# Performance work log

Measured on AMD Instinct MI355X. Metric: run time of the kernel, lower is better.

The kernel has to match this reference:

```python
import jax, jax.numpy as jnp
import numpy as np

B, S, D_IN, D_OUT = 8, 4096, 1024, 1024
R_F, R_M, R_S = 8, 32, 64
R_TOT = R_F + R_M + R_S  # 104
HID = 64
ALPHA = 1.0


def setup_inputs() -> dict:
    key = jax.random.key(0)
    ks = jax.random.split(key, 10)
    inp = {
        "x": jax.random.normal(ks[0], (B, S, D_IN), dtype=jnp.float32),
        # fresh memory state after reset_memory(): zeros of shape [batch, r_*]
        "mem_fast": jnp.zeros((B, R_F), dtype=jnp.float32),
        "mem_medium": jnp.zeros((B, R_M), dtype=jnp.float32),
        "mem_slow": jnp.zeros((B, R_S), dtype=jnp.float32),
        # frozen base nn.Linear
        "base_w": jax.random.normal(ks[1], (D_OUT, D_IN), dtype=jnp.float32) / np.sqrt(D_IN),
        "base_b": jax.random.normal(ks[2], (D_OUT,), dtype=jnp.float32) * 0.01,
        # LoRA projections: proj_down kaiming-ish, proj_up zero-init per _init_weights
        "pd_w": jax.random.normal(ks[3], (R_TOT, D_IN), dtype=jnp.float32) / np.sqrt(D_IN),
        "pu_w": jax.random.normal(ks[4], (D_OUT, R_TOT), dtype=jnp.float32) * 0.01,
        # gate_net: Linear(D_IN, HID) -> GELU -> Linear(HID, 3) -> Softmax
        "g1_w": jax.random.normal(ks[5], (HID, D_IN), dtype=jnp.float32) / np.sqrt(D_IN),
        "g1_b": jnp.zeros((HID,), dtype=jnp.float32),
        "g2_w": jax.random.normal(ks[6], (3, HID), dtype=jnp.float32) / np.sqrt(HID),
        "g2_b": jnp.zeros((3,), dtype=jnp.float32),
    }
    return inp


def reference(x, mem_fast, mem_medium, mem_slow, base_w, base_b,
              pd_w, pu_w, g1_w, g1_b, g2_w, g2_b):
    # base linear: [B,S,D_out]
    base_out = jnp.einsum("bsd,od->bso", x, base_w) + base_b
    # down projection: [B,S,R_TOT]
    proj = jnp.einsum("bsd,rd->bsr", x, pd_w)
    # per-timescale multiplicative modulation by recurrent memory state
    # (split -> (1+mem)*proj -> concat) == concat memories once
    mem = jnp.concatenate([mem_fast, mem_medium, mem_slow], axis=-1)  # [B,R_TOT]
    modulated = proj * (1.0 + mem[:, None, :])
    # gate_net: Linear -> GELU(exact) -> Linear -> softmax over 3 timescales
    h = jax.nn.gelu(jnp.einsum("bsd,hd->bsh", x, g1_w) + g1_b, approximate=False)
    gates = jax.nn.softmax(jnp.einsum("bsh,gh->bsg", h, g2_w) + g2_b, axis=-1)
    gate_scale = jnp.mean(gates, axis=-1, keepdims=True)  # [B,S,1]
    # up projection and residual combine
    lora_out = jnp.einsum("bsr,or->bso", modulated, pu_w)
    output = base_out + ALPHA * lora_out * gate_scale
    return output
```

## Files before the change

kernel.cpp:

```cpp
#include <hip/hip_runtime.h>
#include <stdint.h>


typedef unsigned short ushort_t;
typedef unsigned short us8 __attribute__((ext_vector_type(8)));
typedef short short8 __attribute__((ext_vector_type(8)));
typedef float f32x4 __attribute__((ext_vector_type(4)));

__device__ __forceinline__ ushort_t f2b(float f) {
  union { float f; uint32_t i; } v; v.f = f;
  uint32_t lsb = (v.i >> 16) & 1u;
  v.i += 0x7fffu + lsb;
  return (ushort_t)(v.i >> 16);
}

__device__ __forceinline__ void async16(const void* g, void* l) {
  __builtin_amdgcn_global_load_lds(
      (const __attribute__((address_space(1))) void*)g,
      (__attribute__((address_space(3))) void*)l, 16, 0, 0);
}

__global__ __launch_bounds__(256) void convert_x(const float* __restrict__ x,
                                                 ushort_t* __restrict__ xb) {
  const int flat = blockIdx.x;
  const int b = flat & 7;
  const int c = flat >> 3;
  const size_t i = (((size_t)b * 2048 + c) * 256 + threadIdx.x) * 8;
  f32x4 a0 = *(const f32x4*)(x + i);
  f32x4 a1 = *(const f32x4*)(x + i + 4);
  us8 o;
#pragma unroll
  for (int j = 0; j < 4; j++) { o[j] = f2b(a0[j]); o[4 + j] = f2b(a1[j]); }
  *(us8*)(xb + i) = o;
}

__global__ __launch_bounds__(128) void prep(const float* __restrict__ base_w,
                                            const float* __restrict__ pu_w,
                                            const float* __restrict__ pd_w,
                                            const float* __restrict__ mf,
                                            const float* __restrict__ mm,
                                            const float* __restrict__ ms,
                                            ushort_t* __restrict__ W0,
                                            ushort_t* __restrict__ Weff,
                                            int* __restrict__ flags) {
  const int o = blockIdx.x, y = blockIdx.y, t = threadIdx.x;
  __shared__ float spu[104];
  __shared__ int sflag;
  ushort_t* dst;

  if (y == 0) {
    if (t < 104) spu[t] = pu_w[o * 104 + t] * (1.0f / 3.0f);
    dst = W0 + o * 1024;
    __syncthreads();
  } else {
    const int b = y - 1;
    if (t == 0) sflag = 0;
    __syncthreads();
    float mv = 0.0f;
    if (t < 104) {
      mv = (t < 8) ? mf[b * 8 + t]
         : (t < 40) ? mm[b * 32 + (t - 8)]
                    : ms[b * 64 + (t - 40)];
      if (mv != 0.0f) sflag = 1;
      spu[t] = pu_w[o * 104 + t] * (1.0f + mv) * (1.0f / 3.0f);
    }
    __syncthreads();
    if (o == 0 && t == 0) flags[b] = sflag;
    if (!sflag) return;
    dst = Weff + ((size_t)b << 20) + o * 1024;
  }

  const int d0 = t * 8;
  float acc[8];
  f32x4 b0 = *(const f32x4*)(base_w + o * 1024 + d0);
  f32x4 b1 = *(const f32x4*)(base_w + o * 1024 + d0 + 4);
#pragma unroll
  for (int j = 0; j < 4; j++) { acc[j] = b0[j]; acc[4 + j] = b1[j]; }
  for (int r = 0; r < 104; r++) {
    f32x4 p0 = *(const f32x4*)(pd_w + r * 1024 + d0);
    f32x4 p1 = *(const f32x4*)(pd_w + r * 1024 + d0 + 4);
    float s = spu[r];
#pragma unroll
    for (int j = 0; j < 4; j++) { acc[j] += s * p0[j]; acc[4 + j] += s * p1[j]; }
  }
  us8 ov;
#pragma unroll
  for (int j = 0; j < 8; j++) ov[j] = f2b(acc[j]);
  *(us8*)(dst + d0) = ov;
}

__global__ __launch_bounds__(512, 2) void gemm256(
    const ushort_t* __restrict__ xb, const float* __restrict__ base_b,
    const ushort_t* __restrict__ W0, const ushort_t* __restrict__ Weff,
    const int* __restrict__ flags, float* __restrict__ out) {
  const int flat = blockIdx.x;
  const int b  = flat & 7;
  const int i  = flat >> 3;
  const int bm = i >> 2;
  const int bn = i & 3;

  const ushort_t* W = flags[b] ? (Weff + ((size_t)b << 20)) : W0;

  __shared__ __align__(16) char lds[4 * 32768];

  const int t = threadIdx.x;
  const int w = t >> 6, l = t & 63;
  const int wr = w >> 2, wc = w & 3;
  const int row16 = l & 15, quad = l >> 4;

  const int srow = w * 16 + (l >> 2);
  const int scol = (((l & 3) ^ ((l >> 3) & 3))) * 8;
  const ushort_t* gA = xb + (((size_t)b * 4096 + bm * 256 + srow) << 10) + scol;
  const ushort_t* gB = W + (((size_t)(bn * 256 + srow)) << 10) + scol;

  const int qsw = (quad ^ ((row16 >> 1) & 3)) * 16;
  const int aoff = (wr * 128 + row16) * 64 + qsw;
  const int boff = 16384 + (wc * 64 + row16) * 64 + qsw;

#define STAGE_A(kt)                                                       \
  {                                                                       \
    const int bi_ = (kt) & 3;                                             \
    const ushort_t* g_ = gA + (kt) * 32;                                  \
    char* d_ = lds + bi_ * 32768 + w * 1024;                              \
    async16(g_, d_);                                                      \
    async16(g_ + (128 << 10), d_ + 8192);                                 \
  }
#define STAGE_B(kt)                                                       \
  {                                                                       \
    const int bi_ = (kt) & 3;                                             \
    const ushort_t* g_ = gB + (kt) * 32;                                  \
    char* d_ = lds + bi_ * 32768 + 16384 + w * 1024;                      \
    async16(g_, d_);                                                      \
    async16(g_ + (128 << 10), d_ + 8192);                                 \
  }

  f32x4 acc[8][4] = {};

  STAGE_A(0) STAGE_B(0) STAGE_A(1) STAGE_B(1)
  asm volatile("s_waitcnt vmcnt(4)" ::: "memory");
  __builtin_amdgcn_s_barrier();

  for (int kt = 0; kt < 32; ++kt) {
    const char* base = lds + (kt & 3) * 32768;

    short8 af[8];
#pragma unroll
    for (int mi = 0; mi < 8; ++mi)
      af[mi] = *(const short8*)(base + aoff + mi * 1024);
    short8 bf0 = *(const short8*)(base + boff);
    short8 bf1 = *(const short8*)(base + boff + 1024);
    if (kt < 30) STAGE_A(kt + 2)
    __builtin_amdgcn_s_barrier();
    __builtin_amdgcn_s_setprio(1);
#pragma unroll
    for (int mi = 0; mi < 8; ++mi) {
      acc[mi][0] = __builtin_amdgcn_mfma_f32_16x16x32_bf16(af[mi], bf0, acc[mi][0], 0, 0, 0);
      acc[mi][1] = __builtin_amdgcn_mfma_f32_16x16x32_bf16(af[mi], bf1, acc[mi][1], 0, 0, 0);
    }
    __builtin_amdgcn_s_setprio(0);
    __builtin_amdgcn_s_barrier();

    short8 bf2 = *(const short8*)(base + boff + 2048);
    short8 bf3 = *(const short8*)(base + boff + 3072);
    if (kt < 30) STAGE_B(kt + 2)
    __builtin_amdgcn_s_barrier();
    __builtin_amdgcn_s_setprio(1);
#pragma unroll
    for (int mi = 0; mi < 8; ++mi) {
      acc[mi][2] = __builtin_amdgcn_mfma_f32_16x16x32_bf16(af[mi], bf2, acc[mi][2], 0, 0, 0);
      acc[mi][3] = __builtin_amdgcn_mfma_f32_16x16x32_bf16(af[mi], bf3, acc[mi][3], 0, 0, 0);
    }
    __builtin_amdgcn_s_setprio(0);

    if (kt < 30) {
      asm volatile("s_waitcnt vmcnt(4)" ::: "memory");
    } else if (kt == 30) {
      asm volatile("s_waitcnt vmcnt(0)" ::: "memory");
    }
    __builtin_amdgcn_s_barrier();
  }

#pragma unroll
  for (int ni = 0; ni < 4; ++ni) {
    const int col = bn * 256 + wc * 64 + ni * 16 + row16;
    const float bb = base_b[col];
#pragma unroll
    for (int mi = 0; mi < 8; ++mi) {
      const int row = bm * 256 + wr * 128 + mi * 16 + quad * 4;
      float* po = out + (((size_t)b * 4096 + row) << 10) + col;
#pragma unroll
      for (int i2 = 0; i2 < 4; ++i2)
        po[(size_t)i2 << 10] = acc[mi][ni][i2] + bb;
    }
  }
#undef STAGE_A
#undef STAGE_B
}

extern "C" void kernel_launch(void* const* d_in, const int* in_sizes, int n_in,
                              void* d_out, int out_size, void* d_ws, size_t ws_size,
                              hipStream_t stream) {
  const float* x  = (const float*)d_in[0];
  const float* mf = (const float*)d_in[1];
  const float* mm = (const float*)d_in[2];
  const float* ms = (const float*)d_in[3];
  const float* base_w = (const float*)d_in[4];
  const float* base_b = (const float*)d_in[5];
  const float* pd_w = (const float*)d_in[6];
  const float* pu_w = (const float*)d_in[7];

  char* ws = (char*)d_ws;
  int* flags     = (int*)ws;
  ushort_t* W0   = (ushort_t*)(ws + 4096);
  ushort_t* xb   = (ushort_t*)(ws + 4096 + (2u << 20));
  ushort_t* Weff = (ushort_t*)(ws + 4096 + (2u << 20) + (64u << 20));

  prep<<<dim3(1024, 9), 128, 0, stream>>>(base_w, pu_w, pd_w, mf, mm, ms,
                                          W0, Weff, flags);
  convert_x<<<16384, 256, 0, stream>>>(x, xb);
  gemm256<<<512, 512, 0, stream>>>(xb, base_b, W0, Weff, flags, (float*)d_out);
}
```

Baseline: 347.7 us.

## Double-buffer MFMA fragments in registers and cut GEMM barriers; coarsen convert_x

The GEMM main loop now prefetches the next k-tile's A/B fragments into a second register set while it computes the current one. The M tile is split into two halves of four MFMA rows, so only one barrier per k-step remains instead of four. The vmcnt waits and the placement of STAGE_B are reordered to fit the new schedule. Separately, convert_x processes eight chunks per block with a quarter... rather, an eighth of the blocks, to reduce launch and scheduling overhead. The extra fragment buffers raise register pressure, which could affect the two-blocks-per-CU occupancy.

```diff
diff --git a/kernel.cpp b/kernel.cpp
--- a/kernel.cpp
+++ b/kernel.cpp
@@ -24,14 +24,18 @@
                                                  ushort_t* __restrict__ xb) {
   const int flat = blockIdx.x;
   const int b = flat & 7;
-  const int c = flat >> 3;
-  const size_t i = (((size_t)b * 2048 + c) * 256 + threadIdx.x) * 8;
-  f32x4 a0 = *(const f32x4*)(x + i);
-  f32x4 a1 = *(const f32x4*)(x + i + 4);
-  us8 o;
-#pragma unroll
-  for (int j = 0; j < 4; j++) { o[j] = f2b(a0[j]); o[4 + j] = f2b(a1[j]); }
-  *(us8*)(xb + i) = o;
+  const int c0 = flat >> 3;
+  const size_t base = (size_t)b * 4194304 + (size_t)c0 * 16384;
+#pragma unroll 2
+  for (int u = 0; u < 8; ++u) {
+    const size_t i = base + u * 2048 + threadIdx.x * 8;
+    f32x4 a0 = *(const f32x4*)(x + i);
+    f32x4 a1 = *(const f32x4*)(x + i + 4);
+    us8 o;
+#pragma unroll
+    for (int j = 0; j < 4; j++) { o[j] = f2b(a0[j]); o[4 + j] = f2b(a1[j]); }
+    *(us8*)(xb + i) = o;
+  }
 }
 
 __global__ __launch_bounds__(128) void prep(const float* __restrict__ base_w,
@@ -119,65 +123,75 @@
 
 #define STAGE_A(kt)                                                       \
   {                                                                       \
-    const int bi_ = (kt) & 3;                                             \
     const ushort_t* g_ = gA + (kt) * 32;                                  \
-    char* d_ = lds + bi_ * 32768 + w * 1024;                              \
+    char* d_ = lds + ((kt) & 3) * 32768 + w * 1024;                       \
     async16(g_, d_);                                                      \
     async16(g_ + (128 << 10), d_ + 8192);                                 \
   }
 #define STAGE_B(kt)                                                       \
   {                                                                       \
-    const int bi_ = (kt) & 3;                                             \
     const ushort_t* g_ = gB + (kt) * 32;                                  \
-    char* d_ = lds + bi_ * 32768 + 16384 + w * 1024;                      \
+    char* d_ = lds + ((kt) & 3) * 32768 + 16384 + w * 1024;               \
     async16(g_, d_);                                                      \
     async16(g_ + (128 << 10), d_ + 8192);                                 \
   }
 
   f32x4 acc[8][4] = {};
+  short8 af[2][4], bf[2][4], af2[4];
 
   STAGE_A(0) STAGE_B(0) STAGE_A(1) STAGE_B(1)
   asm volatile("s_waitcnt vmcnt(4)" ::: "memory");
   __builtin_amdgcn_s_barrier();
-
+#pragma unroll
+  for (int mi = 0; mi < 4; ++mi)
+    af[0][mi] = *(const short8*)(lds + aoff + mi * 1024);
+#pragma unroll
+  for (int ni = 0; ni < 4; ++ni)
+    bf[0][ni] = *(const short8*)(lds + boff + ni * 1024);
+
+#pragma unroll 4
   for (int kt = 0; kt < 32; ++kt) {
-    const char* base = lds + (kt & 3) * 32768;
-
-    short8 af[8];
-#pragma unroll
-    for (int mi = 0; mi < 8; ++mi)
-      af[mi] = *(const short8*)(base + aoff + mi * 1024);
-    short8 bf0 = *(const short8*)(base + boff);
-    short8 bf1 = *(const short8*)(base + boff + 1024);
+    const int p = kt & 1;
+    const char* cur = lds + (kt & 3) * 32768;
+    const char* nxt = lds + ((kt + 1) & 3) * 32768;
+
     if (kt < 30) STAGE_A(kt + 2)
-    __builtin_amdgcn_s_barrier();
+#pragma unroll
+    for (int j = 0; j < 4; ++j)
+      af2[j] = *(const short8*)(cur + aoff + (4 + j) * 1024);
     __builtin_amdgcn_s_setprio(1);
 #pragma unroll
-    for (int mi = 0; mi < 8; ++mi) {
-      acc[mi][0] = __builtin_amdgcn_mfma_f32_16x16x32_bf16(af[mi], bf0, acc[mi][0], 0, 0, 0);
-      acc[mi][1] = __builtin_amdgcn_mfma_f32_16x16x32_bf16(af[mi], bf1, acc[mi][1], 0, 0, 0);
-    }
+    for (int mi = 0; mi < 4; ++mi)
+#pragma unroll
+      for (int ni = 0; ni < 4; ++ni)
+        acc[mi][ni] = __builtin_amdgcn_mfma_f32_16x16x32_bf16(af[p][mi], bf[p][ni],
+                                                              acc[mi][ni], 0, 0, 0);
     __builtin_amdgcn_s_setprio(0);
-    __builtin_amdgcn_s_barrier();
-
-    short8 bf2 = *(const short8*)(base + boff + 2048);
-    short8 bf3 = *(const short8*)(base + boff + 3072);
-    if (kt < 30) STAGE_B(kt + 2)
-    __builtin_amdgcn_s_barrier();
-    __builtin_amdgcn_s_setprio(1);
-#pragma unroll
-    for (int mi = 0; mi < 8; ++mi) {
-      acc[mi][2] = __builtin_amdgcn_mfma_f32_16x16x32_bf16(af[mi], bf2, acc[mi][2], 0, 0, 0);
-      acc[mi][3] = __builtin_amdgcn_mfma_f32_16x16x32_bf16(af[mi], bf3, acc[mi][3], 0, 0, 0);
-    }
-    __builtin_amdgcn_s_setprio(0);
 
     if (kt < 30) {
-      asm volatile("s_waitcnt vmcnt(4)" ::: "memory");
+      asm volatile("s_waitcnt vmcnt(2)" ::: "memory");
     } else if (kt == 30) {
       asm volatile("s_waitcnt vmcnt(0)" ::: "memory");
     }
     __builtin_amdgcn_s_barrier();
+
+    if (kt < 30) STAGE_B(kt + 2)
+    if (kt < 31) {
+#pragma unroll
+      for (int mi = 0; mi < 4; ++mi)
+        af[p ^ 1][mi] = *(const short8*)(nxt + aoff + mi * 1024);
+#pragma unroll
+      for (int ni = 0; ni < 4; ++ni)
+        bf[p ^ 1][ni] = *(const short8*)(nxt + boff + ni * 1024);
+    }
+    __builtin_amdgcn_s_setprio(1);
+#pragma unroll
+    for (int mi = 0; mi < 4; ++mi)
+#pragma unroll
+      for (int ni = 0; ni < 4; ++ni)
+        acc[4 + mi][ni] = __builtin_amdgcn_mfma_f32_16x16x32_bf16(af2[mi], bf[p][ni],
+                                                                  acc[4 + mi][ni], 0, 0, 0);
+    __builtin_amdgcn_s_setprio(0);
   }
 
 #pragma unroll
@@ -217,6 +231,6 @@
 
   prep<<<dim3(1024, 9), 128, 0, stream>>>(base_w, pu_w, pd_w, mf, mm, ms,
                                           W0, Weff, flags);
-  convert_x<<<16384, 256, 0, stream>>>(x, xb);
+  convert_x<<<2048, 256, 0, stream>>>(x, xb);
   gemm256<<<512, 512, 0, stream>>>(xb, base_b, W0, Weff, flags, (float*)d_out);
 }
```

New measurement: 408.0 us. 17.3% more time.
